# Kernel optimization log

Hardware: AMD Instinct MI355X
Metric: run time of the kernel (lower is better)

Reference implementation:

```python
import jax, jax.numpy as jnp
import numpy as np

B, C, L, HEADS, DK = 32, 128, 32, 8, 64  # batch, channels, lattice side (L1=L2=L), heads, head dim
NLAYER = 4


def setup_inputs() -> dict:
    key = jax.random.key(0)
    ks = jax.random.split(key, 6)
    s_in = 1.0 / float(np.sqrt(C))          # lecun-normal scale for QKV (fan_in = channels)
    s_out = 1.0 / float(np.sqrt(HEADS * DK))  # lecun-normal scale for W0 (fan_in = dk*heads)
    return {
        "x": jax.random.normal(ks[0], (B, C, L, L), jnp.float32),
        "Wq": jax.random.normal(ks[1], (HEADS * DK, C), jnp.float32) * s_in,
        "Wk": jax.random.normal(ks[2], (HEADS * DK, C), jnp.float32) * s_in,
        "Wv": jax.random.normal(ks[3], (HEADS * DK, C), jnp.float32) * s_in,
        "R": jax.random.normal(ks[4], (HEADS, L, L), jnp.float32) * 0.02,
        "W0": jax.random.normal(ks[5], (C, HEADS * DK), jnp.float32) * s_out,
    }


def get_irpe(R):
    # r[h, i, j] = R[h, (xi - xj) mod L1, (yi - yj) mod L2]  (jnp negative indexing wraps)
    heads, L1, L2 = R.shape
    a1 = jnp.arange(L1)
    a2 = jnp.arange(L2)
    dx = (a1[:, None] - a1[None, :]) % L1        # (L1, L1)
    dy = (a2[:, None] - a2[None, :]) % L2        # (L2, L2)
    bias = R[:, dx[:, None, :, None], dy[None, :, None, :]]  # (heads, L1, L2, L1, L2)
    return bias.reshape(heads, L1 * L2, L1 * L2)


def reference(x, Wq, Wk, Wv, R, W0):
    bias = get_irpe(R)                            # (heads, N, N)
    inv_layer = 1.0 / float(np.sqrt(NLAYER + 1))
    inv_sqrt_dk = 1.0 / float(np.sqrt(DK))

    def block(xs):  # xs: (C, L, L) — single sample, as in the original __call__
        xn = xs * inv_layer
        xf = xn.reshape(C, -1)                    # (C, N)
        Q = (Wq @ xf).reshape(HEADS, DK, -1)      # 1x1 conv == matmul
        K = (Wk @ xf).reshape(HEADS, DK, -1)
        V = (Wv @ xf).reshape(HEADS, DK, -1)
        dot = jnp.einsum('hdi,hdj->hij', Q, K) + bias
        alpha = jax.nn.softmax(dot * inv_sqrt_dk, axis=-1)
        att = jnp.einsum('hij,hdj->hdi', alpha, V).reshape(HEADS * DK, -1)
        return (W0 @ att).reshape(xs.shape) + xs  # residual

    return jax.vmap(block)(x)
```

## Files before the change

kernel.cpp:

```cpp
#include <hip/hip_runtime.h>


#define NB   32
#define NH   8
#define SEQ  1024
#define DKH  64
#define HDIM 512
#define CIN  128

#define SCL 0.18033688011112042f

typedef __bf16 bf16x8 __attribute__((ext_vector_type(8)));
typedef float floatx4 __attribute__((ext_vector_type(4)));
typedef unsigned short u16x8 __attribute__((ext_vector_type(8)));
typedef unsigned int uintx4 __attribute__((ext_vector_type(4)));

__device__ __forceinline__ unsigned short f2bf(float f) {
    union { float f; unsigned int u; } c; c.f = f;
    unsigned int u = c.u;
    return (unsigned short)((u + 0x7fffu + ((u >> 16) & 1u)) >> 16);
}
__device__ __forceinline__ bf16x8 ldfrag(const unsigned short* p) {
    u16x8 v = *reinterpret_cast<const u16x8*>(p);
    return __builtin_bit_cast(bf16x8, v);
}
__device__ __forceinline__ unsigned int pkbf(float a, float b) {
    unsigned int ua = __builtin_bit_cast(unsigned int, a);
    unsigned int ub = __builtin_bit_cast(unsigned int, b);
    ua += 0x7fffu + ((ua >> 16) & 1u);
    ub += 0x7fffu + ((ub >> 16) & 1u);
    return __builtin_amdgcn_perm(ub, ua, 0x07060302u);
}
__device__ __forceinline__ unsigned int pkbf_t(float a, float b) {
    return __builtin_amdgcn_perm(__builtin_bit_cast(unsigned int, b),
                                 __builtin_bit_cast(unsigned int, a), 0x07060302u);
}
__device__ __forceinline__ void g2l16(const void* g, void* l) {
    __builtin_amdgcn_global_load_lds((const __attribute__((address_space(1))) void*)g,
                                     (__attribute__((address_space(3))) void*)l, 16, 0, 0);
}


__global__ __launch_bounds__(256) void prep_all(const float* __restrict__ Wq,
                                                const float* __restrict__ Wk,
                                                const float* __restrict__ Wv,
                                                const float* __restrict__ W0,
                                                const float* __restrict__ R,
                                                const float* __restrict__ x,
                                                unsigned short* __restrict__ w2,
                                                unsigned short* __restrict__ w0f,
                                                float* __restrict__ biasQ4,
                                                unsigned short* __restrict__ xt2) {
    __shared__ float lds[64 * 65];
    int bid = blockIdx.x;
    if (bid < 32) {
        int idx4 = bid * 256 + threadIdx.x;
        int st = idx4 & 31, dxx = (idx4 >> 5) & 31, h = idx4 >> 10;
        const float* Rh = R + (h << 10) + (dxx << 5);
        floatx4 v;
        for (int r = 0; r < 4; ++r) v[r] = Rh[(32 - st - r) & 31] * SCL;
        *(floatx4*)&biasQ4[(size_t)idx4 * 4] = v;
    } else if (bid < 1056) {
        int idx = (bid - 32) * 256 + threadIdx.x;
        if (idx < 196608) {
            int row = idx >> 7, col = idx & 127;
            float v;
            if (row < 512)       v = Wq[idx] * SCL;
            else if (row < 1024) v = Wk[idx - 65536];
            else                 v = Wv[idx - 131072];
            int rt = row >> 4, nr = row & 15, kc = col >> 5, qc = (col & 31) >> 3, jc = col & 7;
            w2[((rt * 4 + kc) * 512) + (qc * 16 + nr) * 8 + jc] = f2bf(v);
        } else {
            int idx2 = idx - 196608;
            int row = idx2 >> 9, col = idx2 & 511;
            int rt = row >> 4, nr = row & 15, kcA = col >> 5, qc = (col & 31) >> 3, jc = col & 7;
            w0f[((rt * 16 + kcA) * 512) + (qc * 16 + nr) * 8 + jc] = f2bf(W0[idx2]);
        }
    } else {
        int r = bid - 1056;
        int b = r & 31, yy = (r >> 5) & 1, zz = r >> 6;
        int c0 = yy * 64, p0 = zz * 64;
        int t = threadIdx.x, tr = t >> 6, tc = t & 63;
        const float inv_layer = 0.44721359549995793f;
        for (int rr = 0; rr < 16; ++rr) {
            int cl = rr * 4 + tr;
            lds[cl * 65 + tc] = x[(b * CIN + c0 + cl) * SEQ + p0 + tc];
        }
        __syncthreads();
        for (int rr = 0; rr < 16; ++rr) {
            int pl = rr * 4 + tr;
            int pos = p0 + pl, c = c0 + tc;
            int pt = pos >> 4, np = pos & 15, kc = c >> 5, qc = (c & 31) >> 3, jc = c & 7;
            xt2[((size_t)((b * 64 + pt) * 4 + kc) * 512) + (qc * 16 + np) * 8 + jc] =
                f2bf(lds[tc * 65 + pl] * inv_layer);
        }
    }
}

__global__ __launch_bounds__(256, 3) void qkv_gemm(const unsigned short* __restrict__ xt2,
                                                   const unsigned short* __restrict__ w2,
                                                   unsigned short* __restrict__ Qt,
                                                   unsigned short* __restrict__ Kf,
                                                   unsigned short* __restrict__ Vf) {
    __shared__ alignas(16) unsigned short lds_s[16 * 512];
    int b = blockIdx.x, y = blockIdx.y, zt = blockIdx.z;
    int tid = threadIdx.x, wave = tid >> 6, lane = tid & 63, q = lane >> 4, n = lane & 15;
    floatx4 acc[4];
    for (int s = 0; s < 4; ++s) acc[s] = (floatx4){0.f, 0.f, 0.f, 0.f};
    bf16x8 af[4];

    if (y < 16) {
        const unsigned short* xsrc = xt2 + (size_t)(b * 64 + zt * 4) * 4 * 512;
        for (int i = 0; i < 4; ++i) {
            int f = wave * 4 + i;
            g2l16(xsrc + f * 512 + lane * 8, &lds_s[f * 512]);
        }
        int rt = y * 4 + wave;
        const unsigned short* wbase = w2 + (size_t)rt * 4 * 512 + lane * 8;
        for (int kc = 0; kc < 4; ++kc) af[kc] = ldfrag(wbase + kc * 512);
        __syncthreads();
#pragma unroll
        for (int kc = 0; kc < 4; ++kc) {
            bf16x8 b0 = ldfrag(&lds_s[(0 * 4 + kc) * 512 + lane * 8]);
            bf16x8 b1 = ldfrag(&lds_s[(1 * 4 + kc) * 512 + lane * 8]);
            bf16x8 b2 = ldfrag(&lds_s[(2 * 4 + kc) * 512 + lane * 8]);
            bf16x8 b3 = ldfrag(&lds_s[(3 * 4 + kc) * 512 + lane * 8]);
            acc[0] = __builtin_amdgcn_mfma_f32_16x16x32_bf16(af[kc], b0, acc[0], 0, 0, 0);
            acc[1] = __builtin_amdgcn_mfma_f32_16x16x32_bf16(af[kc], b1, acc[1], 0, 0, 0);
            acc[2] = __builtin_amdgcn_mfma_f32_16x16x32_bf16(af[kc], b2, acc[2], 0, 0, 0);
            acc[3] = __builtin_amdgcn_mfma_f32_16x16x32_bf16(af[kc], b3, acc[3], 0, 0, 0);
        }
        int wrow0 = y * 64 + wave * 16;
        int pos0 = zt * 64;
        if (y < 8) {
            int h = wrow0 >> 6;
            int d0 = (wrow0 & 63) + 4 * q;
            for (int s = 0; s < 4; ++s) {
                uint2 pk;
                pk.x = pkbf(acc[s][0], acc[s][1]);
                pk.y = pkbf(acc[s][2], acc[s][3]);
                int pos = pos0 + 16 * s + n;
                *(uint2*)&Qt[((size_t)(b * NH + h) * SEQ + pos) * DKH + d0] = pk;
            }
        } else {
            int h = (wrow0 >> 6) - 8;
            int bh = b * NH + h;
            int cd = wave >> 1;
            int qk = 2 * (wave & 1) + (q >> 1);
            int jk = 4 * (q & 1);
            for (int s = 0; s < 4; ++s) {
                uint2 pk;
                pk.x = pkbf(acc[s][0], acc[s][1]);
                pk.y = pkbf(acc[s][2], acc[s][3]);
                size_t addr = ((size_t)(bh * 16 + zt) * 8 + s * 2 + cd) * 512
                              + (qk * 16 + n) * 8 + jk;
                *(uint2*)&Kf[addr] = pk;
            }
        }
    } else {
        const unsigned short* wsrc = w2 + (size_t)(64 + (y - 16) * 4) * 4 * 512;
        for (int i = 0; i < 4; ++i) {
            int f = wave * 4 + i;
            g2l16(wsrc + f * 512 + lane * 8, &lds_s[f * 512]);
        }
        int pt = zt * 4 + wave;
        const unsigned short* xbase = xt2 + (size_t)(b * 64 + pt) * 4 * 512 + lane * 8;
        for (int kc = 0; kc < 4; ++kc) af[kc] = ldfrag(xbase + kc * 512);
        __syncthreads();
#pragma unroll
        for (int kc = 0; kc < 4; ++kc) {
            bf16x8 b0 = ldfrag(&lds_s[(0 * 4 + kc) * 512 + lane * 8]);
            bf16x8 b1 = ldfrag(&lds_s[(1 * 4 + kc) * 512 + lane * 8]);
            bf16x8 b2 = ldfrag(&lds_s[(2 * 4 + kc) * 512 + lane * 8]);
            bf16x8 b3 = ldfrag(&lds_s[(3 * 4 + kc) * 512 + lane * 8]);
            acc[0] = __builtin_amdgcn_mfma_f32_16x16x32_bf16(af[kc], b0, acc[0], 0, 0, 0);
            acc[1] = __builtin_amdgcn_mfma_f32_16x16x32_bf16(af[kc], b1, acc[1], 0, 0, 0);
            acc[2] = __builtin_amdgcn_mfma_f32_16x16x32_bf16(af[kc], b2, acc[2], 0, 0, 0);
            acc[3] = __builtin_amdgcn_mfma_f32_16x16x32_bf16(af[kc], b3, acc[3], 0, 0, 0);
        }
        int vrow0 = (y - 16) * 64;
        int cj = wave >> 1;
        int jj0 = 4 * (wave & 1);
        for (int s = 0; s < 4; ++s) {
            int vrow = vrow0 + 16 * s + n;
            int h = vrow >> 6, d = vrow & 63;
            int u = d >> 4, nl = d & 15;
            uint2 pk;
            pk.x = pkbf(acc[s][0], acc[s][1]);
            pk.y = pkbf(acc[s][2], acc[s][3]);
            size_t addr = ((size_t)((b * NH + h) * 16 + zt) * 8 + u * 2 + cj) * 512
                          + (q * 16 + nl) * 8 + jj0;
            *(uint2*)&Vf[addr] = pk;
        }
    }
}

__global__ __launch_bounds__(256, 2) void attn_kernel(const unsigned short* __restrict__ Qt,
                                                      const unsigned short* __restrict__ Kf,
                                                      const unsigned short* __restrict__ Vf,
                                                      const float* __restrict__ biasQ4,
                                                      unsigned short* __restrict__ att2) {
    __shared__ alignas(16) unsigned short lds_k[2][8 * 512];
    __shared__ alignas(16) unsigned short lds_v[2][8 * 512];
    __shared__ alignas(16) float lds_bQ[4096];

    int gid = blockIdx.x;
    int bh = gid & 255, qb = gid >> 8;
    int b = bh >> 3, h = bh & 7;
    int tid = threadIdx.x, wave = tid >> 6, lane = tid & 63, q = lane >> 4, n = lane & 15;
    int i0 = qb * 256 + wave * 64;
    int ti0 = i0 >> 4;

    const unsigned short* qbase = Qt + (size_t)bh * SEQ * DKH;
    const unsigned short* kft = Kf + (size_t)bh * 16 * 4096;
    const unsigned short* vft = Vf + (size_t)bh * 16 * 4096;
    int off0 = wave * 512;

    {
        const float* bQg = biasQ4 + (size_t)h * 4096;
        for (int i = 0; i < 4; ++i) {
            int fo = i * 1024 + wave * 256;
            g2l16(bQg + fo + lane * 4, &lds_bQ[fo]);
        }
        g2l16(kft + off0 + lane * 8,        &lds_k[0][off0]);
        g2l16(kft + 2048 + off0 + lane * 8, &lds_k[0][2048 + off0]);
        g2l16(vft + off0 + lane * 8,        &lds_v[0][off0]);
        g2l16(vft + 2048 + off0 + lane * 8, &lds_v[0][2048 + off0]);
    }

    bf16x8 aq[4][2];
    for (int qt = 0; qt < 4; ++qt)
        for (int c = 0; c < 2; ++c)
            aq[qt][c] = ldfrag(qbase + (i0 + 16 * qt + n) * DKH + c * 32 + q * 8);

    floatx4 o[4][4];
    float lsum[4] = {0.f, 0.f, 0.f, 0.f};
    for (int qt = 0; qt < 4; ++qt)
        for (int u = 0; u < 4; ++u) o[qt][u] = (floatx4){0.f, 0.f, 0.f, 0.f};

    int st0_4 = ((4 * q - n) & 31) * 4;
    int st1_4 = (((4 * q - n) + 16) & 31) * 4;
    int ee64 = qb * 8 + 2 * wave + 256;

    __syncthreads();

#define LDB(qt, s0, s1, s2, s3) do {                                          \
        int eh_ = ee64 + ((qt) >> 1);                                         \
        int dh_ = (eh_ & 31) << 7;                                            \
        int dl_ = ((eh_ - 1) & 31) << 7;                                      \
        int sa_ = ((qt) & 1) ? st1_4 : st0_4;                                 \
        int sb_ = ((qt) & 1) ? st0_4 : st1_4;                                 \
        s0 = *(const floatx4*)&lds_bQ[dh_ + sa_];                             \
        s1 = *(const floatx4*)&lds_bQ[dh_ + sb_];                             \
        s2 = *(const floatx4*)&lds_bQ[dl_ + sa_];                             \
        s3 = *(const floatx4*)&lds_bQ[dl_ + sb_];                             \
    } while (0)

#define SMM(qt, s0, s1, s2, s3) do {                                          \
        s0 = __builtin_amdgcn_mfma_f32_16x16x32_bf16(kf2[0][0], aq[qt][0], s0, 0, 0, 0); \
        s0 = __builtin_amdgcn_mfma_f32_16x16x32_bf16(kf2[0][1], aq[qt][1], s0, 0, 0, 0); \
        s1 = __builtin_amdgcn_mfma_f32_16x16x32_bf16(kf2[1][0], aq[qt][0], s1, 0, 0, 0); \
        s1 = __builtin_amdgcn_mfma_f32_16x16x32_bf16(kf2[1][1], aq[qt][1], s1, 0, 0, 0); \
        s2 = __builtin_amdgcn_mfma_f32_16x16x32_bf16(kf2[2][0], aq[qt][0], s2, 0, 0, 0); \
        s2 = __builtin_amdgcn_mfma_f32_16x16x32_bf16(kf2[2][1], aq[qt][1], s2, 0, 0, 0); \
        s3 = __builtin_amdgcn_mfma_f32_16x16x32_bf16(kf2[3][0], aq[qt][0], s3, 0, 0, 0); \
        s3 = __builtin_amdgcn_mfma_f32_16x16x32_bf16(kf2[3][1], aq[qt][1], s3, 0, 0, 0); \
    } while (0)

#define EPO(qt, s0, s1, s2, s3) do {                                          \
        floatx4 e0_, e1_, e2_, e3_;                                           \
        for (int r_ = 0; r_ < 4; ++r_) {                                      \
            e0_[r_] = __builtin_amdgcn_exp2f(s0[r_]);                         \
            e1_[r_] = __builtin_amdgcn_exp2f(s1[r_]);                         \
            e2_[r_] = __builtin_amdgcn_exp2f(s2[r_]);                         \
            e3_[r_] = __builtin_amdgcn_exp2f(s3[r_]);                         \
        }                                                                     \
        uintx4 pu0_, pu1_;                                                    \
        pu0_[0] = pkbf_t(e0_[0], e0_[1]);                                     \
        pu0_[1] = pkbf_t(e0_[2], e0_[3]);                                     \
        pu0_[2] = pkbf_t(e1_[0], e1_[1]);                                     \
        pu0_[3] = pkbf_t(e1_[2], e1_[3]);                                     \
        pu1_[0] = pkbf_t(e2_[0], e2_[1]);                                     \
        pu1_[1] = pkbf_t(e2_[2], e2_[3]);                                     \
        pu1_[2] = pkbf_t(e3_[0], e3_[1]);                                     \
        pu1_[3] = pkbf_t(e3_[2], e3_[3]);                                     \
        bf16x8 pf0_ = __builtin_bit_cast(bf16x8, pu0_);                       \
        bf16x8 pf1_ = __builtin_bit_cast(bf16x8, pu1_);                       \
        floatx4 es_ = (e0_ + e1_) + (e2_ + e3_);                              \
        lsum[qt] += (es_[0] + es_[1]) + (es_[2] + es_[3]);                    \
        o[qt][0] = __builtin_amdgcn_mfma_f32_16x16x32_bf16(vf2[0][0], pf0_, o[qt][0], 0, 0, 0); \
        o[qt][0] = __builtin_amdgcn_mfma_f32_16x16x32_bf16(vf2[0][1], pf1_, o[qt][0], 0, 0, 0); \
        o[qt][1] = __builtin_amdgcn_mfma_f32_16x16x32_bf16(vf2[1][0], pf0_, o[qt][1], 0, 0, 0); \
        o[qt][1] = __builtin_amdgcn_mfma_f32_16x16x32_bf16(vf2[1][1], pf1_, o[qt][1], 0, 0, 0); \
        o[qt][2] = __builtin_amdgcn_mfma_f32_16x16x32_bf16(vf2[2][0], pf0_, o[qt][2], 0, 0, 0); \
        o[qt][2] = __builtin_amdgcn_mfma_f32_16x16x32_bf16(vf2[2][1], pf1_, o[qt][2], 0, 0, 0); \
        o[qt][3] = __builtin_amdgcn_mfma_f32_16x16x32_bf16(vf2[3][0], pf0_, o[qt][3], 0, 0, 0); \
        o[qt][3] = __builtin_amdgcn_mfma_f32_16x16x32_bf16(vf2[3][1], pf1_, o[qt][3], 0, 0, 0); \
    } while (0)

    for (int kt = 0; kt < 16; ++kt) {
        int cur = kt & 1;

        if (kt < 15) {
            const unsigned short* kg = kft + (kt + 1) * 4096;
            const unsigned short* vg = vft + (kt + 1) * 4096;
            unsigned short* dk = &lds_k[cur ^ 1][0];
            unsigned short* dv = &lds_v[cur ^ 1][0];
            g2l16(kg + off0 + lane * 8,        dk + off0);
            g2l16(kg + 2048 + off0 + lane * 8, dk + 2048 + off0);
            g2l16(vg + off0 + lane * 8,        dv + off0);
            g2l16(vg + 2048 + off0 + lane * 8, dv + 2048 + off0);
        }

        bf16x8 kf2[4][2], vf2[4][2];
#pragma unroll
        for (int s = 0; s < 4; ++s)
#pragma unroll
            for (int c = 0; c < 2; ++c) {
                kf2[s][c] = ldfrag(&lds_k[cur][(s * 2 + c) * 512 + lane * 8]);
                vf2[s][c] = ldfrag(&lds_v[cur][(s * 2 + c) * 512 + lane * 8]);
            }

        floatx4 s0, s1, s2, s3;
        LDB(0, s0, s1, s2, s3);
        SMM(0, s0, s1, s2, s3);
        EPO(0, s0, s1, s2, s3);
        LDB(1, s0, s1, s2, s3);
        SMM(1, s0, s1, s2, s3);
        EPO(1, s0, s1, s2, s3);
        LDB(2, s0, s1, s2, s3);
        SMM(2, s0, s1, s2, s3);
        EPO(2, s0, s1, s2, s3);
        LDB(3, s0, s1, s2, s3);
        SMM(3, s0, s1, s2, s3);
        EPO(3, s0, s1, s2, s3);

        ee64 -= 2;
        __syncthreads();
    }

#undef LDB
#undef SMM
#undef EPO

    for (int qt = 0; qt < 4; ++qt) {
        float ls = lsum[qt];
        ls += __shfl_xor(ls, 16, 64);
        ls += __shfl_xor(ls, 32, 64);
        float inv = 1.0f / ls;
        int pt = ti0 + qt;
        for (int u = 0; u < 4; ++u) {
            int kcA = 2 * h + (u >> 1);
            int q2 = 2 * (u & 1) + (q >> 1);
            uint2 pk;
            pk.x = pkbf(o[qt][u][0] * inv, o[qt][u][1] * inv);
            pk.y = pkbf(o[qt][u][2] * inv, o[qt][u][3] * inv);
            size_t addr = ((size_t)((b * 64 + pt) * 16 + kcA) * 512)
                          + (q2 * 16 + n) * 8 + 4 * (q & 1);
            *(uint2*)&att2[addr] = pk;
        }
    }
}

__global__ __launch_bounds__(256, 3) void out_gemm(const unsigned short* __restrict__ att2,
                                                   const unsigned short* __restrict__ w0f,
                                                   const float* __restrict__ x,
                                                   float* __restrict__ out) {
    __shared__ alignas(16) unsigned short lds_w[2][16 * 512];
    int b = blockIdx.x, ct = blockIdx.y, ptb = blockIdx.z;
    int tid = threadIdx.x, wave = tid >> 6, lane = tid & 63, q = lane >> 4, n = lane & 15;
    int pos0 = ptb * 64 + wave * 16;
    int c0 = ct * 64;
    int pt = ptb * 4 + wave;
    const unsigned short* abase = att2 + (size_t)(b * 64 + pt) * 16 * 512 + lane * 8;
    const unsigned short* wsrc = w0f + (size_t)(c0 >> 4) * 16 * 512;
    floatx4 acc[4];
    for (int s = 0; s < 4; ++s) acc[s] = (floatx4){0.f, 0.f, 0.f, 0.f};

    for (int k2 = 0; k2 < 4; ++k2)
        g2l16(wsrc + (wave * 16 + k2) * 512 + lane * 8, &lds_w[0][(wave * 4 + k2) * 512]);
    __syncthreads();

    for (int g = 0; g < 4; ++g) {
        int buf = g & 1;
        if (g < 3) {
            for (int k2 = 0; k2 < 4; ++k2)
                g2l16(wsrc + (wave * 16 + (g + 1) * 4 + k2) * 512 + lane * 8,
                      &lds_w[buf ^ 1][(wave * 4 + k2) * 512]);
        }
        bf16x8 af[4];
        for (int k2 = 0; k2 < 4; ++k2) af[k2] = ldfrag(abase + (g * 4 + k2) * 512);
#pragma unroll
        for (int k2 = 0; k2 < 4; ++k2) {
            bf16x8 b0 = ldfrag(&lds_w[buf][(0 * 4 + k2) * 512 + lane * 8]);
            bf16x8 b1 = ldfrag(&lds_w[buf][(1 * 4 + k2) * 512 + lane * 8]);
            bf16x8 b2 = ldfrag(&lds_w[buf][(2 * 4 + k2) * 512 + lane * 8]);
            bf16x8 b3 = ldfrag(&lds_w[buf][(3 * 4 + k2) * 512 + lane * 8]);
            acc[0] = __builtin_amdgcn_mfma_f32_16x16x32_bf16(af[k2], b0, acc[0], 0, 0, 0);
            acc[1] = __builtin_amdgcn_mfma_f32_16x16x32_bf16(af[k2], b1, acc[1], 0, 0, 0);
            acc[2] = __builtin_amdgcn_mfma_f32_16x16x32_bf16(af[k2], b2, acc[2], 0, 0, 0);
            acc[3] = __builtin_amdgcn_mfma_f32_16x16x32_bf16(af[k2], b3, acc[3], 0, 0, 0);
        }
        __syncthreads();
    }

    int p0q = pos0 + 4 * q;
    for (int s = 0; s < 4; ++s) {
        int c = c0 + 16 * s + n;
        size_t idx = ((size_t)b * CIN + c) * SEQ + p0q;
        floatx4 res = *(const floatx4*)&x[idx];
        floatx4 v = acc[s] + res;
        *(floatx4*)&out[idx] = v;
    }
}

extern "C" void kernel_launch(void* const* d_in, const int* in_sizes, int n_in,
                              void* d_out, int out_size, void* d_ws, size_t ws_size,
                              hipStream_t stream) {
    const float* x  = (const float*)d_in[0];
    const float* Wq = (const float*)d_in[1];
    const float* Wk = (const float*)d_in[2];
    const float* Wv = (const float*)d_in[3];
    const float* R  = (const float*)d_in[4];
    const float* W0 = (const float*)d_in[5];
    float* out = (float*)d_out;

    char* ws = (char*)d_ws;
    size_t off = 0;
    unsigned short* Qt   = (unsigned short*)(ws + off); off += (size_t)NB * NH * SEQ * DKH * 2;
    unsigned short* Kf   = (unsigned short*)(ws + off); off += (size_t)NB * NH * SEQ * DKH * 2;
    unsigned short* Vf   = (unsigned short*)(ws + off); off += (size_t)NB * NH * SEQ * DKH * 2;
    unsigned short* att2 = (unsigned short*)(ws + off); off += (size_t)NB * SEQ * HDIM * 2;
    unsigned short* xt2  = (unsigned short*)(ws + off); off += (size_t)NB * SEQ * CIN * 2;
    unsigned short* w2   = (unsigned short*)(ws + off); off += (size_t)1536 * 128 * 2;
    unsigned short* w0f  = (unsigned short*)(ws + off); off += (size_t)128 * 512 * 2;
    float* biasQ4 = (float*)(ws + off); off += (size_t)NH * 32 * 32 * 4 * 4;
    (void)ws_size; (void)in_sizes; (void)n_in; (void)out_size;

    prep_all<<<2080, 256, 0, stream>>>(Wq, Wk, Wv, W0, R, x, w2, w0f, biasQ4, xt2);
    qkv_gemm<<<dim3(NB, 24, 16), 256, 0, stream>>>(xt2, w2, Qt, Kf, Vf);
    attn_kernel<<<NB * NH * 4, 256, 0, stream>>>(Qt, Kf, Vf, biasQ4, att2);
    out_gemm<<<dim3(NB, 2, 16), 256, 0, stream>>>(att2, w0f, x, out);
}
```

Baseline: 192.0 us.

## Fuse QKV output tiles into one block reusing x fragments in registers

The QKV GEMM no longer launches one block per 64-row output tile. Each block now loads its 64-position x tile into LDS once, keeps all 16 fragments in registers, and loops over all Q, K and V row tiles. This cuts redundant x loads and the grid size from 12288 to 512 blocks. In exchange there is less parallelism (512 blocks, 2 per CU by launch bounds), higher register pressure, and the V weights are read straight from global memory without LDS staging.

```diff
diff --git a/kernel.cpp b/kernel.cpp
--- a/kernel.cpp
+++ b/kernel.cpp
@@ -97,57 +97,78 @@
     }
 }
 
-__global__ __launch_bounds__(256, 3) void qkv_gemm(const unsigned short* __restrict__ xt2,
+__global__ __launch_bounds__(256, 2) void qkv_gemm(const unsigned short* __restrict__ xt2,
                                                    const unsigned short* __restrict__ w2,
                                                    unsigned short* __restrict__ Qt,
                                                    unsigned short* __restrict__ Kf,
                                                    unsigned short* __restrict__ Vf) {
     __shared__ alignas(16) unsigned short lds_s[16 * 512];
-    int b = blockIdx.x, y = blockIdx.y, zt = blockIdx.z;
+    int b = blockIdx.x, zt = blockIdx.y;
     int tid = threadIdx.x, wave = tid >> 6, lane = tid & 63, q = lane >> 4, n = lane & 15;
-    floatx4 acc[4];
-    for (int s = 0; s < 4; ++s) acc[s] = (floatx4){0.f, 0.f, 0.f, 0.f};
-    bf16x8 af[4];
-
-    if (y < 16) {
-        const unsigned short* xsrc = xt2 + (size_t)(b * 64 + zt * 4) * 4 * 512;
-        for (int i = 0; i < 4; ++i) {
-            int f = wave * 4 + i;
-            g2l16(xsrc + f * 512 + lane * 8, &lds_s[f * 512]);
-        }
+
+    const unsigned short* xsrc = xt2 + (size_t)(b * 64 + zt * 4) * 4 * 512;
+    for (int i = 0; i < 4; ++i) {
+        int f = wave * 4 + i;
+        g2l16(xsrc + f * 512 + lane * 8, &lds_s[f * 512]);
+    }
+    __syncthreads();
+
+    bf16x8 xf[16];
+#pragma unroll
+    for (int f = 0; f < 16; ++f) xf[f] = ldfrag(&lds_s[f * 512 + lane * 8]);
+
+    int bh0 = b * NH;
+    int pos0 = zt * 64;
+
+    for (int y = 0; y < 8; ++y) {
         int rt = y * 4 + wave;
         const unsigned short* wbase = w2 + (size_t)rt * 4 * 512 + lane * 8;
+        bf16x8 af[4];
+#pragma unroll
         for (int kc = 0; kc < 4; ++kc) af[kc] = ldfrag(wbase + kc * 512);
-        __syncthreads();
-#pragma unroll
-        for (int kc = 0; kc < 4; ++kc) {
-            bf16x8 b0 = ldfrag(&lds_s[(0 * 4 + kc) * 512 + lane * 8]);
-            bf16x8 b1 = ldfrag(&lds_s[(1 * 4 + kc) * 512 + lane * 8]);
-            bf16x8 b2 = ldfrag(&lds_s[(2 * 4 + kc) * 512 + lane * 8]);
-            bf16x8 b3 = ldfrag(&lds_s[(3 * 4 + kc) * 512 + lane * 8]);
-            acc[0] = __builtin_amdgcn_mfma_f32_16x16x32_bf16(af[kc], b0, acc[0], 0, 0, 0);
-            acc[1] = __builtin_amdgcn_mfma_f32_16x16x32_bf16(af[kc], b1, acc[1], 0, 0, 0);
-            acc[2] = __builtin_amdgcn_mfma_f32_16x16x32_bf16(af[kc], b2, acc[2], 0, 0, 0);
-            acc[3] = __builtin_amdgcn_mfma_f32_16x16x32_bf16(af[kc], b3, acc[3], 0, 0, 0);
-        }
+        floatx4 acc[4];
+#pragma unroll
+        for (int s = 0; s < 4; ++s) acc[s] = (floatx4){0.f, 0.f, 0.f, 0.f};
+#pragma unroll
+        for (int kc = 0; kc < 4; ++kc)
+#pragma unroll
+            for (int s = 0; s < 4; ++s)
+                acc[s] = __builtin_amdgcn_mfma_f32_16x16x32_bf16(af[kc], xf[s * 4 + kc], acc[s], 0, 0, 0);
         int wrow0 = y * 64 + wave * 16;
-        int pos0 = zt * 64;
-        if (y < 8) {
-            int h = wrow0 >> 6;
-            int d0 = (wrow0 & 63) + 4 * q;
-            for (int s = 0; s < 4; ++s) {
-                uint2 pk;
-                pk.x = pkbf(acc[s][0], acc[s][1]);
-                pk.y = pkbf(acc[s][2], acc[s][3]);
-                int pos = pos0 + 16 * s + n;
-                *(uint2*)&Qt[((size_t)(b * NH + h) * SEQ + pos) * DKH + d0] = pk;
-            }
-        } else {
+        int h = wrow0 >> 6;
+        int d0 = (wrow0 & 63) + 4 * q;
+#pragma unroll
+        for (int s = 0; s < 4; ++s) {
+            uint2 pk;
+            pk.x = pkbf(acc[s][0], acc[s][1]);
+            pk.y = pkbf(acc[s][2], acc[s][3]);
+            int pos = pos0 + 16 * s + n;
+            *(uint2*)&Qt[((size_t)(bh0 + h) * SEQ + pos) * DKH + d0] = pk;
+        }
+    }
+
+    {
+        int cd = wave >> 1;
+        int qk = 2 * (wave & 1) + (q >> 1);
+        int jk = 4 * (q & 1);
+        for (int y = 8; y < 16; ++y) {
+            int rt = y * 4 + wave;
+            const unsigned short* wbase = w2 + (size_t)rt * 4 * 512 + lane * 8;
+            bf16x8 af[4];
+#pragma unroll
+            for (int kc = 0; kc < 4; ++kc) af[kc] = ldfrag(wbase + kc * 512);
+            floatx4 acc[4];
+#pragma unroll
+            for (int s = 0; s < 4; ++s) acc[s] = (floatx4){0.f, 0.f, 0.f, 0.f};
+#pragma unroll
+            for (int kc = 0; kc < 4; ++kc)
+#pragma unroll
+                for (int s = 0; s < 4; ++s)
+                    acc[s] = __builtin_amdgcn_mfma_f32_16x16x32_bf16(af[kc], xf[s * 4 + kc], acc[s], 0, 0, 0);
+            int wrow0 = y * 64 + wave * 16;
             int h = (wrow0 >> 6) - 8;
-            int bh = b * NH + h;
-            int cd = wave >> 1;
-            int qk = 2 * (wave & 1) + (q >> 1);
-            int jk = 4 * (q & 1);
+            int bh = bh0 + h;
+#pragma unroll
             for (int s = 0; s < 4; ++s) {
                 uint2 pk;
                 pk.x = pkbf(acc[s][0], acc[s][1]);
@@ -157,40 +178,43 @@
                 *(uint2*)&Kf[addr] = pk;
             }
         }
-    } else {
-        const unsigned short* wsrc = w2 + (size_t)(64 + (y - 16) * 4) * 4 * 512;
-        for (int i = 0; i < 4; ++i) {
-            int f = wave * 4 + i;
-            g2l16(wsrc + f * 512 + lane * 8, &lds_s[f * 512]);
-        }
-        int pt = zt * 4 + wave;
-        const unsigned short* xbase = xt2 + (size_t)(b * 64 + pt) * 4 * 512 + lane * 8;
-        for (int kc = 0; kc < 4; ++kc) af[kc] = ldfrag(xbase + kc * 512);
-        __syncthreads();
-#pragma unroll
-        for (int kc = 0; kc < 4; ++kc) {
-            bf16x8 b0 = ldfrag(&lds_s[(0 * 4 + kc) * 512 + lane * 8]);
-            bf16x8 b1 = ldfrag(&lds_s[(1 * 4 + kc) * 512 + lane * 8]);
-            bf16x8 b2 = ldfrag(&lds_s[(2 * 4 + kc) * 512 + lane * 8]);
-            bf16x8 b3 = ldfrag(&lds_s[(3 * 4 + kc) * 512 + lane * 8]);
-            acc[0] = __builtin_amdgcn_mfma_f32_16x16x32_bf16(af[kc], b0, acc[0], 0, 0, 0);
-            acc[1] = __builtin_amdgcn_mfma_f32_16x16x32_bf16(af[kc], b1, acc[1], 0, 0, 0);
-            acc[2] = __builtin_amdgcn_mfma_f32_16x16x32_bf16(af[kc], b2, acc[2], 0, 0, 0);
-            acc[3] = __builtin_amdgcn_mfma_f32_16x16x32_bf16(af[kc], b3, acc[3], 0, 0, 0);
-        }
-        int vrow0 = (y - 16) * 64;
+    }
+
+    {
         int cj = wave >> 1;
         int jj0 = 4 * (wave & 1);
-        for (int s = 0; s < 4; ++s) {
-            int vrow = vrow0 + 16 * s + n;
-            int h = vrow >> 6, d = vrow & 63;
-            int u = d >> 4, nl = d & 15;
-            uint2 pk;
-            pk.x = pkbf(acc[s][0], acc[s][1]);
-            pk.y = pkbf(acc[s][2], acc[s][3]);
-            size_t addr = ((size_t)((b * NH + h) * 16 + zt) * 8 + u * 2 + cj) * 512
-                          + (q * 16 + nl) * 8 + jj0;
-            *(uint2*)&Vf[addr] = pk;
+        bf16x8 xa0 = xf[wave * 4 + 0], xa1 = xf[wave * 4 + 1];
+        bf16x8 xa2 = xf[wave * 4 + 2], xa3 = xf[wave * 4 + 3];
+        for (int yv = 0; yv < 8; ++yv) {
+            const unsigned short* wbase = w2 + (size_t)(64 + yv * 4) * 4 * 512 + lane * 8;
+            floatx4 acc[4];
+#pragma unroll
+            for (int s = 0; s < 4; ++s) acc[s] = (floatx4){0.f, 0.f, 0.f, 0.f};
+#pragma unroll
+            for (int kc = 0; kc < 4; ++kc) {
+                bf16x8 a_ = (kc == 0) ? xa0 : (kc == 1) ? xa1 : (kc == 2) ? xa2 : xa3;
+                bf16x8 b0 = ldfrag(wbase + (0 * 4 + kc) * 512);
+                bf16x8 b1 = ldfrag(wbase + (1 * 4 + kc) * 512);
+                bf16x8 b2 = ldfrag(wbase + (2 * 4 + kc) * 512);
+                bf16x8 b3 = ldfrag(wbase + (3 * 4 + kc) * 512);
+                acc[0] = __builtin_amdgcn_mfma_f32_16x16x32_bf16(a_, b0, acc[0], 0, 0, 0);
+                acc[1] = __builtin_amdgcn_mfma_f32_16x16x32_bf16(a_, b1, acc[1], 0, 0, 0);
+                acc[2] = __builtin_amdgcn_mfma_f32_16x16x32_bf16(a_, b2, acc[2], 0, 0, 0);
+                acc[3] = __builtin_amdgcn_mfma_f32_16x16x32_bf16(a_, b3, acc[3], 0, 0, 0);
+            }
+            int vrow0 = yv * 64;
+#pragma unroll
+            for (int s = 0; s < 4; ++s) {
+                int vrow = vrow0 + 16 * s + n;
+                int h = vrow >> 6, d = vrow & 63;
+                int u = d >> 4, nl = d & 15;
+                uint2 pk;
+                pk.x = pkbf(acc[s][0], acc[s][1]);
+                pk.y = pkbf(acc[s][2], acc[s][3]);
+                size_t addr = ((size_t)((bh0 + h) * 16 + zt) * 8 + u * 2 + cj) * 512
+                              + (q * 16 + nl) * 8 + jj0;
+                *(uint2*)&Vf[addr] = pk;
+            }
         }
     }
 }
@@ -438,7 +462,7 @@
     (void)ws_size; (void)in_sizes; (void)n_in; (void)out_size;
 
     prep_all<<<2080, 256, 0, stream>>>(Wq, Wk, Wv, W0, R, x, w2, w0f, biasQ4, xt2);
-    qkv_gemm<<<dim3(NB, 24, 16), 256, 0, stream>>>(xt2, w2, Qt, Kf, Vf);
+    qkv_gemm<<<dim3(NB, 16), 256, 0, stream>>>(xt2, w2, Qt, Kf, Vf);
     attn_kernel<<<NB * NH * 4, 256, 0, stream>>>(Qt, Kf, Vf, biasQ4, att2);
     out_gemm<<<dim3(NB, 2, 16), 256, 0, stream>>>(att2, w0f, x, out);
 }
```

Result: slower. 202.3 us (+5.3%).
